# Kernel tuning notes

Hardware: AMD Instinct MI355X
Metric: run time of the kernel (lower is better)

The kernel has to match this reference:

```python
import jax, jax.numpy as jnp
import numpy as np

CELL = 14
NC = 80
BPC = 3
IMG = 448.0
CS = IMG / CELL  # cell pixel size
CLASS_SCALE = 1.0
OBJECT_SCALE = 1.0
NOOBJECT_SCALE = 0.5
COORD_SCALE = 5.0
EPS = 1e-9

# base_boxes[y, x, b, :] = (x*CS, y*CS, 0, 0)
_gy, _gx = jnp.meshgrid(jnp.arange(CELL, dtype=jnp.float32), jnp.arange(CELL, dtype=jnp.float32), indexing='ij')
BASE = jnp.broadcast_to(jnp.stack([_gx * CS, _gy * CS, jnp.zeros_like(_gx), jnp.zeros_like(_gx)], axis=-1)[:, :, None, :], (CELL, CELL, BPC, 4))
MULT = jnp.array([CS, CS, IMG, IMG], dtype=jnp.float32)


def _ciou(boxes1, box2):
    # boxes1: [S,S,BPC,4] (cx,cy,w,h); box2: [4]
    b1_cx, b1_cy, b1_w, b1_h = boxes1[..., 0], boxes1[..., 1], boxes1[..., 2], boxes1[..., 3]
    b2_cx, b2_cy, b2_w, b2_h = box2[0], box2[1], box2[2], box2[3]
    b1_x1, b1_y1, b1_x2, b1_y2 = b1_cx - b1_w / 2, b1_cy - b1_h / 2, b1_cx + b1_w / 2, b1_cy + b1_h / 2
    b2_x1, b2_y1, b2_x2, b2_y2 = b2_cx - b2_w / 2, b2_cy - b2_h / 2, b2_cx + b2_w / 2, b2_cy + b2_h / 2
    inter = jnp.clip(jnp.minimum(b1_x2, b2_x2) - jnp.maximum(b1_x1, b2_x1), 0) * \
            jnp.clip(jnp.minimum(b1_y2, b2_y2) - jnp.maximum(b1_y1, b2_y1), 0)
    union = b1_w * b1_h + b2_w * b2_h - inter
    iou = inter / (union + EPS)
    center_distance = (b1_cx - b2_cx) ** 2 + (b1_cy - b2_cy) ** 2
    # faithful to original (uses center/size components for the enclosing box)
    enclose_left = jnp.minimum(boxes1[..., 0], box2[0])
    enclose_right = jnp.maximum(boxes1[..., 2], box2[2])
    enclose_top = jnp.minimum(boxes1[..., 1], box2[1])
    enclose_bottom = jnp.maximum(boxes1[..., 3], box2[3])
    enclose_diag = (enclose_right - enclose_left) ** 2 + (enclose_bottom - enclose_top) ** 2
    v = (4.0 / jnp.pi ** 2) * (jnp.arctan(b2_w / (b2_h + EPS)) - jnp.arctan(b1_w / (b1_h + EPS))) ** 2
    alpha = jax.lax.stop_gradient(v / (1 - iou + v + EPS))
    return iou - center_distance / (enclose_diag + EPS) - alpha * v  # [S,S,BPC]


def _l2(t):
    return 0.5 * jnp.sum(t * t)


def _per_object_loss(predict, label):
    # predict: [S,S,NC+5*BPC], label: [5]
    gy = jnp.arange(CELL, dtype=jnp.float32)[:, None]
    gx = jnp.arange(CELL, dtype=jnp.float32)[None, :]
    x, y, w, h = label[0], label[1], label[2], label[3]
    min_x = jnp.floor((x - w / 2) / CS)
    max_x = jnp.minimum(jnp.ceil((x + w / 2) / CS), CELL)
    min_y = jnp.floor((y - h / 2) / CS)
    max_y = jnp.minimum(jnp.ceil((y + h / 2) / CS), CELL)
    object_mask = ((gx >= min_x) & (gx < max_x) & (gy >= min_y) & (gy < max_y)).astype(jnp.float32)
    cx, cy = jnp.floor(x / CS), jnp.floor(y / CS)
    center_mask = ((gx == cx) & (gy == cy)).astype(jnp.float32)

    pboxes = predict[:, :, NC + BPC:].reshape(CELL, CELL, BPC, 4) * MULT + BASE
    iou = _ciou(pboxes, label[:4])                     # [S,S,BPC]
    C = iou * center_mask[..., None]
    I = (iou >= jnp.max(iou, axis=-1, keepdims=True)).astype(jnp.float32) * center_mask[..., None]
    no_I = 1.0 - I
    p_C = predict[:, :, NC:NC + BPC]

    sqrt_w, sqrt_h = jnp.sqrt(jnp.abs(w)), jnp.sqrt(jnp.abs(h))
    p_x, p_y = pboxes[..., 0], pboxes[..., 1]
    p_sqrt_w = jnp.sqrt(jnp.clip(pboxes[..., 2], 0.0, IMG))
    p_sqrt_h = jnp.sqrt(jnp.clip(pboxes[..., 3], 0.0, IMG))

    P = jax.nn.one_hot(label[4].astype(jnp.int32), NC, dtype=jnp.float32)
    p_P = predict[:, :, :NC]

    class_loss = _l2(object_mask[..., None] * (p_P - P)) * CLASS_SCALE
    object_loss = _l2(I * (p_C - C)) * OBJECT_SCALE
    noobject_loss = _l2(no_I * p_C) * NOOBJECT_SCALE
    coord_loss = (_l2(I * (p_x - x) / CS) + _l2(I * (p_y - y) / CS)
                  + _l2(I * (p_sqrt_w - sqrt_w)) / IMG + _l2(I * (p_sqrt_h - sqrt_h)) / IMG) * COORD_SCALE
    return class_loss + object_loss + noobject_loss + coord_loss


def setup_inputs() -> dict:
    key = jax.random.key(0)
    k1, k2, k3, k4, k5 = jax.random.split(key, 5)
    B, M = 1024, 30
    predicts = jax.random.normal(k1, (B, CELL, CELL, NC + 5 * BPC), dtype=jnp.float32) * 0.1
    xy = jax.random.uniform(k2, (B, M, 2), minval=60.0, maxval=IMG - 60.0)
    wh = jax.random.uniform(k3, (B, M, 2), minval=10.0, maxval=100.0)
    cls = jax.random.randint(k4, (B, M, 1), 0, NC).astype(jnp.float32)
    labels = jnp.concatenate([xy, wh, cls], axis=-1)
    objects_num = jax.random.randint(k5, (B,), 1, M + 1).astype(jnp.int32)
    return {"predicts": predicts, "labels": labels, "objects_num": objects_num}


def reference(predicts, labels, objects_num):
    B, M = labels.shape[0], labels.shape[1]
    per_batch = jax.vmap(lambda p, ls: jax.vmap(lambda l: _per_object_loss(p, l))(ls))
    losses = per_batch(predicts, labels)  # [B, M]
    mask = (jnp.arange(M)[None, :] < objects_num[:, None]).astype(jnp.float32)
    return jnp.sum(losses * mask) / B
```

## Files before the change

### kernel.cpp

```cpp
#include <hip/hip_runtime.h>
#include <math.h>

#define CELLN 14
#define NCELLS 196
#define NCLS 80
#define NCH 95
#define NDW (NCELLS * NCH)
#define NF4 (NDW / 4)

__global__ __launch_bounds__(256) void yolo_loss_kernel(
    const float* __restrict__ predicts,
    const float* __restrict__ labels,
    const int* __restrict__ objects_num,
    float* __restrict__ out,
    int M, float invB)
{
    __shared__ float s_pP[NCELLS * NCLS];
    __shared__ float s_classSS[NCELLS];
    __shared__ float s_red[8];

    const int img  = blockIdx.x;
    const int tid  = threadIdx.x;
    const int lane = tid & 63;
    const int wid  = tid >> 6;

    const float* gpred = predicts + (size_t)img * NDW;
    const float4* gp4  = (const float4*)gpred;

    float pc2 = 0.0f;
    #pragma unroll
    for (int i = 0; i < 19; ++i) {
        int f = tid + (i << 8);
        if (f < NF4) {
            float4 v4 = gp4[f];
            unsigned idx  = (unsigned)f << 2;
            unsigned cell = idx / 95u;
            unsigned ch   = idx - cell * 95u;
            float vv[4] = {v4.x, v4.y, v4.z, v4.w};
            #pragma unroll
            for (int k = 0; k < 4; ++k) {
                if (ch < (unsigned)NCLS) {
                    s_pP[cell * NCLS + ch] = vv[k];
                } else if (ch < 83u) {
                    pc2 += vv[k] * vv[k];
                }
                ++ch;
                if (ch == 95u) { ch = 0u; ++cell; }
            }
        }
    }

    #pragma unroll
    for (int off = 32; off; off >>= 1) pc2 += __shfl_down(pc2, off);
    if (lane == 0) s_red[wid] = pc2;
    __syncthreads();
    const float S_pC2 = s_red[0] + s_red[1] + s_red[2] + s_red[3];

    {
        const int sub  = tid & 15;
        const int cl16 = tid >> 4;
        for (int c0 = 0; c0 < NCELLS; c0 += 16) {
            int cell = c0 + cl16;
            float a = 0.0f;
            if (cell < NCELLS) {
                #pragma unroll
                for (int j = 0; j < 5; ++j) {
                    float v = s_pP[cell * NCLS + sub + 16 * j];
                    a += v * v;
                }
            }
            #pragma unroll
            for (int off = 8; off; off >>= 1) a += __shfl_xor(a, off, 16);
            if (sub == 0 && cell < NCELLS) s_classSS[cell] = a;
        }
    }
    __syncthreads();

    float acc = 0.0f;
    const int g = tid >> 3;
    const int r = tid & 7;
    const int n = objects_num[img];
    if (g < n) {
        const float* lab = labels + ((size_t)img * M + g) * 5;
        const float x = lab[0], y = lab[1], w = lab[2], h = lab[3];
        const int cls = (int)lab[4];
        const float inv32 = 1.0f / 32.0f;

        int min_x = max(0, (int)floorf((x - w * 0.5f) * inv32));
        int max_x = min(CELLN, (int)ceilf((x + w * 0.5f) * inv32));
        int min_y = max(0, (int)floorf((y - h * 0.5f) * inv32));
        int max_y = min(CELLN, (int)ceilf((y + h * 0.5f) * inv32));
        int nx = max_x - min_x;
        int ncell = nx * (max_y - min_y);

        float csum = 0.0f;
        for (int p = r; p < ncell; p += 8) {
            int gy = min_y + p / nx;
            int gx = min_x + p % nx;
            int cell = gy * CELLN + gx;
            csum += s_classSS[cell] - 2.0f * s_pP[cell * NCLS + cls] + 1.0f;
        }
        acc = 0.5f * csum;

        if (r == 0) {
            int cx = (int)floorf(x * inv32);
            int cy = (int)floorf(y * inv32);
            int ccell = cy * CELLN + cx;
            const float* cp = gpred + ccell * NCH;
            float bx = (float)cx * 32.0f;
            float by = (float)cy * 32.0f;

            float pC[3], ciou[3], pxv[3], pyv[3], pwv[3], phv[3];
            #pragma unroll
            for (int b = 0; b < 3; ++b) {
                pC[b] = cp[NCLS + b];
                float px = cp[83 + 4*b] * 32.0f + bx;
                float py = cp[84 + 4*b] * 32.0f + by;
                float pw = cp[85 + 4*b] * 448.0f;
                float ph = cp[86 + 4*b] * 448.0f;
                pxv[b] = px; pyv[b] = py; pwv[b] = pw; phv[b] = ph;
                float iw = fminf(px + pw*0.5f, x + w*0.5f) - fmaxf(px - pw*0.5f, x - w*0.5f);
                float ih = fminf(py + ph*0.5f, y + h*0.5f) - fmaxf(py - ph*0.5f, y - h*0.5f);
                iw = fmaxf(iw, 0.0f); ih = fmaxf(ih, 0.0f);
                float inter = iw * ih;
                float uni = pw*ph + w*h - inter;
                float iou = inter / (uni + 1e-9f);
                float cd = (px - x)*(px - x) + (py - y)*(py - y);
                float el = fminf(px, x), er = fmaxf(pw, w);
                float et = fminf(py, y), eb = fmaxf(ph, h);
                float ed = (er - el)*(er - el) + (eb - et)*(eb - et);
                float da = atanf(w / (h + 1e-9f)) - atanf(pw / (ph + 1e-9f));
                float v = 0.40528473456935108577f * da * da;
                float alpha = v / (1.0f - iou + v + 1e-9f);
                ciou[b] = iou - cd / (ed + 1e-9f) - alpha * v;
            }
            float mx = fmaxf(ciou[0], fmaxf(ciou[1], ciou[2]));
            float sqw = sqrtf(fabsf(w)), sqh = sqrtf(fabsf(h));
            float sel_obj = 0.0f, sel_pc2 = 0.0f, coord = 0.0f;
            #pragma unroll
            for (int b = 0; b < 3; ++b) {
                if (ciou[b] >= mx) {
                    float d = pC[b] - ciou[b];
                    sel_obj += d * d;
                    sel_pc2 += pC[b] * pC[b];
                    float dx = (pxv[b] - x) * inv32;
                    float dy = (pyv[b] - y) * inv32;
                    float psw = sqrtf(fminf(fmaxf(pwv[b], 0.0f), 448.0f));
                    float psh = sqrtf(fminf(fmaxf(phv[b], 0.0f), 448.0f));
                    float dw = psw - sqw, dh = psh - sqh;
                    coord += dx*dx + dy*dy + (dw*dw + dh*dh) * (1.0f/448.0f);
                }
            }
            acc += 0.5f * sel_obj + 0.25f * (S_pC2 - sel_pc2) + 2.5f * coord;
        }
    }

    #pragma unroll
    for (int off = 32; off; off >>= 1) acc += __shfl_down(acc, off);
    if (lane == 0) s_red[wid] = acc;
    __syncthreads();
    if (tid == 0) {
        atomicAdd(out, (s_red[0] + s_red[1] + s_red[2] + s_red[3]) * invB);
    }
}

extern "C" void kernel_launch(void* const* d_in, const int* in_sizes, int n_in,
                              void* d_out, int out_size, void* d_ws, size_t ws_size,
                              hipStream_t stream) {
    const float* predicts = (const float*)d_in[0];
    const float* labels   = (const float*)d_in[1];
    const int*   objn     = (const int*)d_in[2];
    float* out = (float*)d_out;

    const int B = in_sizes[2];
    const int M = in_sizes[1] / (B * 5);

    yolo_loss_kernel<<<dim3(B), dim3(256), 0, stream>>>(
        predicts, labels, objn, out, M, 1.0f / (float)B);
}
```

Baseline: 138.9 us.

## Scatter per-cell object counts and class weights before streaming predictions

Reverses the order of work: objects first scatter per-cell coverage counts and packed 8-bit per-class hit counts into shared memory with atomics. The prediction stream then folds the class loss directly as 0.5*cnt*v^2 - wgt*v, so the 62KB shared staging buffer, the per-cell sum-of-squares pass and one barrier are no longer needed. This cuts shared memory sharply, which may raise occupancy, but it adds shared atomics and relies on per-cell class counts fitting in 8 bits.

```diff
diff --git a/kernel.cpp b/kernel.cpp
--- a/kernel.cpp
+++ b/kernel.cpp
@@ -7,6 +7,7 @@
 #define NCH 95
 #define NDW (NCELLS * NCH)
 #define NF4 (NDW / 4)
+#define NW32 (NCELLS * 20)
 
 __global__ __launch_bounds__(256) void yolo_loss_kernel(
     const float* __restrict__ predicts,
@@ -15,17 +16,48 @@
     float* __restrict__ out,
     int M, float invB)
 {
-    __shared__ float s_pP[NCELLS * NCLS];
-    __shared__ float s_classSS[NCELLS];
-    __shared__ float s_red[8];
+    __shared__ unsigned s_W32[NW32];
+    __shared__ float    s_cnt[NCELLS];
+    __shared__ float    s_red[4];
 
     const int img  = blockIdx.x;
     const int tid  = threadIdx.x;
     const int lane = tid & 63;
     const int wid  = tid >> 6;
+    const float inv32 = 1.0f / 32.0f;
 
-    const float* gpred = predicts + (size_t)img * NDW;
-    const float4* gp4  = (const float4*)gpred;
+    const float*  gpred = predicts + (size_t)img * NDW;
+    const float4* gp4   = (const float4*)gpred;
+    const int n = objects_num[img];
+
+    for (int i = tid; i < NW32; i += 256) s_W32[i] = 0u;
+    for (int i = tid; i < NCELLS; i += 256) s_cnt[i] = 0.0f;
+    __syncthreads();
+
+    float acc = 0.0f;
+    for (int g = (tid >> 3); g < n; g += 32) {
+        const int r = tid & 7;
+        const float* lab = labels + ((size_t)img * M + g) * 5;
+        const float x = lab[0], y = lab[1], w = lab[2], h = lab[3];
+        const int cls = (int)lab[4];
+
+        int min_x = max(0, (int)floorf((x - w * 0.5f) * inv32));
+        int max_x = min(CELLN, (int)ceilf((x + w * 0.5f) * inv32));
+        int min_y = max(0, (int)floorf((y - h * 0.5f) * inv32));
+        int max_y = min(CELLN, (int)ceilf((y + h * 0.5f) * inv32));
+        int nx = max_x - min_x;
+        int ncell = nx * (max_y - min_y);
+
+        if (r == 0) acc += 0.5f * (float)ncell;
+        const unsigned winc = 1u << (8 * (cls & 3));
+        const int      woff = cls >> 2;
+        for (int p = r; p < ncell; p += 8) {
+            int cell = (min_y + p / nx) * CELLN + (min_x + p % nx);
+            atomicAdd(&s_cnt[cell], 1.0f);
+            atomicAdd(&s_W32[cell * 20 + woff], winc);
+        }
+    }
+    __syncthreads();
 
     float pc2 = 0.0f;
     #pragma unroll
@@ -39,120 +71,73 @@
             float vv[4] = {v4.x, v4.y, v4.z, v4.w};
             #pragma unroll
             for (int k = 0; k < 4; ++k) {
+                float v = vv[k];
                 if (ch < (unsigned)NCLS) {
-                    s_pP[cell * NCLS + ch] = vv[k];
+                    unsigned wword = s_W32[cell * 20 + (ch >> 2)];
+                    float wgt = (float)((wword >> (8 * (ch & 3))) & 255u);
+                    acc += 0.5f * s_cnt[cell] * v * v - wgt * v;
                 } else if (ch < 83u) {
-                    pc2 += vv[k] * vv[k];
+                    pc2 += v * v;
                 }
                 ++ch;
                 if (ch == 95u) { ch = 0u; ++cell; }
             }
         }
     }
+    acc += 0.25f * (float)n * pc2;
 
-    #pragma unroll
-    for (int off = 32; off; off >>= 1) pc2 += __shfl_down(pc2, off);
-    if (lane == 0) s_red[wid] = pc2;
-    __syncthreads();
-    const float S_pC2 = s_red[0] + s_red[1] + s_red[2] + s_red[3];
+    for (int o = tid; o < n; o += 256) {
+        const float* lab = labels + ((size_t)img * M + o) * 5;
+        const float x = lab[0], y = lab[1], w = lab[2], h = lab[3];
 
-    {
-        const int sub  = tid & 15;
-        const int cl16 = tid >> 4;
-        for (int c0 = 0; c0 < NCELLS; c0 += 16) {
-            int cell = c0 + cl16;
-            float a = 0.0f;
-            if (cell < NCELLS) {
-                #pragma unroll
-                for (int j = 0; j < 5; ++j) {
-                    float v = s_pP[cell * NCLS + sub + 16 * j];
-                    a += v * v;
-                }
+        int cx = (int)floorf(x * inv32);
+        int cy = (int)floorf(y * inv32);
+        const float* cp = gpred + (cy * CELLN + cx) * NCH;
+        float bx = (float)cx * 32.0f;
+        float by = (float)cy * 32.0f;
+
+        float pC[3], ciou[3], pxv[3], pyv[3], pwv[3], phv[3];
+        #pragma unroll
+        for (int b = 0; b < 3; ++b) {
+            pC[b] = cp[NCLS + b];
+            float px = cp[83 + 4*b] * 32.0f + bx;
+            float py = cp[84 + 4*b] * 32.0f + by;
+            float pw = cp[85 + 4*b] * 448.0f;
+            float ph = cp[86 + 4*b] * 448.0f;
+            pxv[b] = px; pyv[b] = py; pwv[b] = pw; phv[b] = ph;
+            float iw = fminf(px + pw*0.5f, x + w*0.5f) - fmaxf(px - pw*0.5f, x - w*0.5f);
+            float ih = fminf(py + ph*0.5f, y + h*0.5f) - fmaxf(py - ph*0.5f, y - h*0.5f);
+            iw = fmaxf(iw, 0.0f); ih = fmaxf(ih, 0.0f);
+            float inter = iw * ih;
+            float uni = pw*ph + w*h - inter;
+            float iou = inter / (uni + 1e-9f);
+            float cd = (px - x)*(px - x) + (py - y)*(py - y);
+            float el = fminf(px, x), er = fmaxf(pw, w);
+            float et = fminf(py, y), eb = fmaxf(ph, h);
+            float ed = (er - el)*(er - el) + (eb - et)*(eb - et);
+            float da = atanf(w / (h + 1e-9f)) - atanf(pw / (ph + 1e-9f));
+            float v = 0.40528473456935108577f * da * da;
+            float alpha = v / (1.0f - iou + v + 1e-9f);
+            ciou[b] = iou - cd / (ed + 1e-9f) - alpha * v;
+        }
+        float mx = fmaxf(ciou[0], fmaxf(ciou[1], ciou[2]));
+        float sqw = sqrtf(fabsf(w)), sqh = sqrtf(fabsf(h));
+        float sel_obj = 0.0f, sel_pc2 = 0.0f, coord = 0.0f;
+        #pragma unroll
+        for (int b = 0; b < 3; ++b) {
+            if (ciou[b] >= mx) {
+                float d = pC[b] - ciou[b];
+                sel_obj += d * d;
+                sel_pc2 += pC[b] * pC[b];
+                float dx = (pxv[b] - x) * inv32;
+                float dy = (pyv[b] - y) * inv32;
+                float psw = sqrtf(fminf(fmaxf(pwv[b], 0.0f), 448.0f));
+                float psh = sqrtf(fminf(fmaxf(phv[b], 0.0f), 448.0f));
+                float dw = psw - sqw, dh = psh - sqh;
+                coord += dx*dx + dy*dy + (dw*dw + dh*dh) * (1.0f/448.0f);
             }
-            #pragma unroll
-            for (int off = 8; off; off >>= 1) a += __shfl_xor(a, off, 16);
-            if (sub == 0 && cell < NCELLS) s_classSS[cell] = a;
         }
-    }
-    __syncthreads();
-
-    float acc = 0.0f;
-    const int g = tid >> 3;
-    const int r = tid & 7;
-    const int n = objects_num[img];
-    if (g < n) {
-        const float* lab = labels + ((size_t)img * M + g) * 5;
-        const float x = lab[0], y = lab[1], w = lab[2], h = lab[3];
-        const int cls = (int)lab[4];
-        const float inv32 = 1.0f / 32.0f;
-
-        int min_x = max(0, (int)floorf((x - w * 0.5f) * inv32));
-        int max_x = min(CELLN, (int)ceilf((x + w * 0.5f) * inv32));
-        int min_y = max(0, (int)floorf((y - h * 0.5f) * inv32));
-        int max_y = min(CELLN, (int)ceilf((y + h * 0.5f) * inv32));
-        int nx = max_x - min_x;
-        int ncell = nx * (max_y - min_y);
-
-        float csum = 0.0f;
-        for (int p = r; p < ncell; p += 8) {
-            int gy = min_y + p / nx;
-            int gx = min_x + p % nx;
-            int cell = gy * CELLN + gx;
-            csum += s_classSS[cell] - 2.0f * s_pP[cell * NCLS + cls] + 1.0f;
-        }
-        acc = 0.5f * csum;
-
-        if (r == 0) {
-            int cx = (int)floorf(x * inv32);
-            int cy = (int)floorf(y * inv32);
-            int ccell = cy * CELLN + cx;
-            const float* cp = gpred + ccell * NCH;
-            float bx = (float)cx * 32.0f;
-            float by = (float)cy * 32.0f;
-
-            float pC[3], ciou[3], pxv[3], pyv[3], pwv[3], phv[3];
-            #pragma unroll
-            for (int b = 0; b < 3; ++b) {
-                pC[b] = cp[NCLS + b];
-                float px = cp[83 + 4*b] * 32.0f + bx;
-                float py = cp[84 + 4*b] * 32.0f + by;
-                float pw = cp[85 + 4*b] * 448.0f;
-                float ph = cp[86 + 4*b] * 448.0f;
-                pxv[b] = px; pyv[b] = py; pwv[b] = pw; phv[b] = ph;
-                float iw = fminf(px + pw*0.5f, x + w*0.5f) - fmaxf(px - pw*0.5f, x - w*0.5f);
-                float ih = fminf(py + ph*0.5f, y + h*0.5f) - fmaxf(py - ph*0.5f, y - h*0.5f);
-                iw = fmaxf(iw, 0.0f); ih = fmaxf(ih, 0.0f);
-                float inter = iw * ih;
-                float uni = pw*ph + w*h - inter;
-                float iou = inter / (uni + 1e-9f);
-                float cd = (px - x)*(px - x) + (py - y)*(py - y);
-                float el = fminf(px, x), er = fmaxf(pw, w);
-                float et = fminf(py, y), eb = fmaxf(ph, h);
-                float ed = (er - el)*(er - el) + (eb - et)*(eb - et);
-                float da = atanf(w / (h + 1e-9f)) - atanf(pw / (ph + 1e-9f));
-                float v = 0.40528473456935108577f * da * da;
-                float alpha = v / (1.0f - iou + v + 1e-9f);
-                ciou[b] = iou - cd / (ed + 1e-9f) - alpha * v;
-            }
-            float mx = fmaxf(ciou[0], fmaxf(ciou[1], ciou[2]));
-            float sqw = sqrtf(fabsf(w)), sqh = sqrtf(fabsf(h));
-            float sel_obj = 0.0f, sel_pc2 = 0.0f, coord = 0.0f;
-            #pragma unroll
-            for (int b = 0; b < 3; ++b) {
-                if (ciou[b] >= mx) {
-                    float d = pC[b] - ciou[b];
-                    sel_obj += d * d;
-                    sel_pc2 += pC[b] * pC[b];
-                    float dx = (pxv[b] - x) * inv32;
-                    float dy = (pyv[b] - y) * inv32;
-                    float psw = sqrtf(fminf(fmaxf(pwv[b], 0.0f), 448.0f));
-                    float psh = sqrtf(fminf(fmaxf(phv[b], 0.0f), 448.0f));
-                    float dw = psw - sqw, dh = psh - sqh;
-                    coord += dx*dx + dy*dy + (dw*dw + dh*dh) * (1.0f/448.0f);
-                }
-            }
-            acc += 0.5f * sel_obj + 0.25f * (S_pC2 - sel_pc2) + 2.5f * coord;
-        }
+        acc += 0.5f * sel_obj - 0.25f * sel_pc2 + 2.5f * coord;
     }
 
     #pragma unroll
```

Result: faster. 119.5 us (-13.9%).
